# Kernel optimization log

Hardware: AMD Instinct MI355X
Metric: run time of the kernel (lower is better)

The kernel has to match this reference:

```python
import jax, jax.numpy as jnp
import numpy as np


def setup_inputs() -> dict:
    key = jax.random.key(0)
    k1, k2, k3 = jax.random.split(key, 3)
    num, c_in, c_out, nx, ny, din, dout = 128, 3, 8, 31, 31, 4, 6
    x = jax.random.normal(k1, (num, c_in, din, nx + 1, ny + 1), dtype=jnp.float32)
    tensors = jax.random.normal(k2, (c_in, c_out, nx, ny, din, din, din, din, dout), dtype=jnp.float32)
    bias = jax.random.normal(k3, (c_out, nx, ny, dout), dtype=jnp.float32) * 1e-8
    return {"x": x, "tensors": tensors, "bias": bias}


def reference(x, tensors, bias):
    # x: [num, c_in, din, sx, sy]; tensors: [c_in, c_out, nx, ny, din,din,din,din, dout]
    num, c_in, din, sx, sy = x.shape
    X, Y = sx - 1, sy - 1  # == nx, ny
    c_out, dout = tensors.shape[1], tensors.shape[-1]
    # four 2x2-patch corners, each [num, c_in, din, X, Y]
    a = x[:, :, :, :-1, :-1]
    b = x[:, :, :, 1:, :-1]
    c = x[:, :, :, :-1, 1:]
    d = x[:, :, :, 1:, 1:]
    # outer product of the four corner vectors -> rank-4 local feature [num, c_in, din^4, X, Y]
    ab = jnp.einsum('ncixy,ncjxy->ncijxy', a, b)
    cd = jnp.einsum('nckxy,nclxy->ncklxy', c, d)
    patch = jnp.einsum('ncijxy,ncklxy->ncijklxy', ab, cd)
    patch = patch.reshape(num, c_in, din ** 4, X, Y)
    # per-position weight: [c_in, c_out, X, Y, din^4, dout]
    w = tensors.reshape(c_in, c_out, X, Y, din ** 4, dout)
    out = jnp.einsum('ncmxy,cpxymo->npoxy', patch, w)  # [num, c_out, dout, X, Y]
    out = out + bias.transpose(0, 3, 1, 2)[None]  # bias -> [1, c_out, dout, X, Y]
    return out
```

## Files before the change

### kernel.cpp

```cpp
#include <hip/hip_runtime.h>


typedef __attribute__((ext_vector_type(8))) short short8;
typedef __attribute__((ext_vector_type(4))) float floatx4;
typedef __attribute__((ext_vector_type(4))) unsigned int uintx4;

#define WS_ELEMS (961u * 6144u)
#define SA_STR 72
#define SW_STR 72

static __device__ __forceinline__ unsigned short f2bf(float f) {
  union { float f; unsigned u; } v; v.f = f;
  unsigned r = v.u + 0x7FFFu + ((v.u >> 16) & 1u);
  return (unsigned short)(r >> 16);
}

template <bool TO_WS>
__global__ __launch_bounds__(256, 4)
void ttn_conv_mfma(const float* __restrict__ x,
                   const float* __restrict__ tensors,
                   const float* __restrict__ bias,
                   float* __restrict__ dst) {
  __shared__ __align__(16) unsigned short sA[128 * SA_STR];
  __shared__ __align__(16) unsigned short sW[48 * SW_STR];

  const int site = blockIdx.x;
  const int xx = site / 31, yy = site - xx * 31;
  const int t = threadIdx.x;
  const int lane = t & 63, wave = t >> 6;
  const int row = lane & 15, quad = lane >> 4;

  const int n_st = t & 127;
  const int h = t >> 7;
  const int p_st = t >> 5;
  const int q_st = t & 31;

  floatx4 acc[2][3];
#pragma unroll
  for (int i0 = 0; i0 < 2; ++i0)
#pragma unroll
    for (int j0 = 0; j0 < 3; ++j0)
      acc[i0][j0] = (floatx4){0.f, 0.f, 0.f, 0.f};

  float areg[4], b0 = 0.f, b1 = 0.f, cdreg[16];
  float4 wv0, wv1, wv2;

  {
    const float* src = tensors + ((size_t)(p_st * 961 + site)) * 1536 + 12 * q_st;
    wv0 = *(const float4*)src;
    wv1 = *(const float4*)(src + 4);
    wv2 = *(const float4*)(src + 8);
  }

#pragma unroll
  for (int ch = 0; ch < 12; ++ch) {
    const int mb = ch & 3;
    if ((ch & 3) == 0) {
      const int c = ch >> 2;
      const float* xp = x + ((size_t)n_st * 3 + c) * 4096 + xx * 32 + yy;
      float bq[4], cq[4], dq[4];
#pragma unroll
      for (int i = 0; i < 4; ++i) {
        const float* r0 = xp + i * 1024;
        areg[i] = r0[0];
        cq[i]   = r0[1];
        bq[i]   = r0[32];
        dq[i]   = r0[33];
      }
      b0 = h ? bq[2] : bq[0];
      b1 = h ? bq[3] : bq[1];
#pragma unroll
      for (int k2 = 0; k2 < 4; ++k2)
#pragma unroll
        for (int l2 = 0; l2 < 4; ++l2)
          cdreg[k2 * 4 + l2] = cq[k2] * dq[l2];
    }
    __syncthreads();

    {
      const float vv[12] = {wv0.x, wv0.y, wv0.z, wv0.w, wv1.x, wv1.y,
                            wv1.z, wv1.w, wv2.x, wv2.y, wv2.z, wv2.w};
#pragma unroll
      for (int o = 0; o < 6; ++o) {
        const unsigned pk = (unsigned)f2bf(vv[o]) | ((unsigned)f2bf(vv[o + 6]) << 16);
        *(unsigned*)&sW[(p_st * 6 + o) * SW_STR + 2 * q_st] = pk;
      }
    }
#pragma unroll
    for (int e = 0; e < 2; ++e) {
      const float ab = areg[mb] * (e ? b1 : b0);
      unsigned pk[8];
#pragma unroll
      for (int u = 0; u < 8; ++u)
        pk[u] = (unsigned)f2bf(ab * cdreg[2 * u]) |
                ((unsigned)f2bf(ab * cdreg[2 * u + 1]) << 16);
      uintx4* dp = (uintx4*)&sA[n_st * SA_STR + (2 * h + e) * 16];
      uintx4 v0 = {pk[0], pk[1], pk[2], pk[3]};
      uintx4 v1 = {pk[4], pk[5], pk[6], pk[7]};
      dp[0] = v0;
      dp[1] = v1;
    }
    if (ch < 11) {
      const int cn = (ch + 1) >> 2, mbn = (ch + 1) & 3;
      const float* src = tensors +
          ((size_t)((cn * 8 + p_st) * 961 + site)) * 1536 + (mbn * 64 + 2 * q_st) * 6;
      wv0 = *(const float4*)src;
      wv1 = *(const float4*)(src + 4);
      wv2 = *(const float4*)(src + 8);
    }
    __syncthreads();

#pragma unroll
    for (int ks = 0; ks < 2; ++ks) {
      const int kof = ks * 32 + quad * 8;
      short8 af[2], bf[3];
#pragma unroll
      for (int mt = 0; mt < 2; ++mt)
        af[mt] = *(const short8*)&sA[(wave * 32 + mt * 16 + row) * SA_STR + kof];
#pragma unroll
      for (int nt = 0; nt < 3; ++nt)
        bf[nt] = *(const short8*)&sW[(nt * 16 + row) * SW_STR + kof];
#pragma unroll
      for (int mt = 0; mt < 2; ++mt)
#pragma unroll
        for (int nt = 0; nt < 3; ++nt)
          acc[mt][nt] = __builtin_amdgcn_mfma_f32_16x16x32_bf16(
              af[mt], bf[nt], acc[mt][nt], 0, 0, 0);
    }
  }

  if (TO_WS) {
#pragma unroll
    for (int mt = 0; mt < 2; ++mt)
#pragma unroll
      for (int r = 0; r < 4; ++r) {
        const int n = wave * 32 + mt * 16 + quad * 4 + r;
#pragma unroll
        for (int nt = 0; nt < 3; ++nt) {
          const int po = nt * 16 + row;
          dst[(size_t)site * 6144 + n * 48 + po] = acc[mt][nt][r];
        }
      }
  } else {
#pragma unroll
    for (int mt = 0; mt < 2; ++mt)
#pragma unroll
      for (int r = 0; r < 4; ++r) {
        const int n = wave * 32 + mt * 16 + quad * 4 + r;
#pragma unroll
        for (int nt = 0; nt < 3; ++nt) {
          const int po = nt * 16 + row;
          const int p = po / 6, o = po - p * 6;
          dst[(size_t)(n * 48 + po) * 961 + site] =
              acc[mt][nt][r] + bias[(p * 961 + site) * 6 + o];
        }
      }
  }
}

__global__ __launch_bounds__(256, 8)
void ttn_transpose_bias(const float* __restrict__ ws,
                        const float* __restrict__ bias,
                        float* __restrict__ out) {
  __shared__ float tile[32][33];
  const int f0 = blockIdx.x * 32;
  const int s0 = blockIdx.y * 32;
  const int tx = threadIdx.x;
  const int ty = threadIdx.y;

#pragma unroll
  for (int rr = 0; rr < 4; ++rr) {
    const int srow = ty + rr * 8;
    const int site = s0 + srow;
    if (site < 961)
      tile[srow][tx] = ws[(size_t)site * 6144 + f0 + tx];
  }
  __syncthreads();

#pragma unroll
  for (int rr = 0; rr < 4; ++rr) {
    const int fy = ty + rr * 8;
    const int f = f0 + fy;
    const int site = s0 + tx;
    if (site < 961) {
      const int po = f % 48;
      const int p = po / 6, o = po - p * 6;
      out[(size_t)f * 961 + site] = tile[tx][fy] + bias[(p * 961 + site) * 6 + o];
    }
  }
}

extern "C" void kernel_launch(void* const* d_in, const int* in_sizes, int n_in,
                              void* d_out, int out_size, void* d_ws, size_t ws_size,
                              hipStream_t stream) {
  const float* x       = (const float*)d_in[0];
  const float* tensors = (const float*)d_in[1];
  const float* bias    = (const float*)d_in[2];
  float* out           = (float*)d_out;

  const size_t need = (size_t)WS_ELEMS * sizeof(float);
  if (d_ws != nullptr && ws_size >= need) {
    float* ws = (float*)d_ws;
    hipLaunchKernelGGL((ttn_conv_mfma<true>), dim3(961), dim3(256), 0, stream,
                       x, tensors, bias, ws);
    hipLaunchKernelGGL(ttn_transpose_bias, dim3(192, 31), dim3(32, 8), 0, stream,
                       ws, bias, out);
  } else {
    hipLaunchKernelGGL((ttn_conv_mfma<false>), dim3(961), dim3(256), 0, stream,
                       x, tensors, bias, out);
  }
}
```

Baseline: 244.8 us.

## Build patch A-fragments in registers and double-buffer weight tiles in LDS

The shared-memory staging of the outer-product patch matrix is removed. Each lane now computes its own bf16 A-fragment directly in registers from per-row corner values that it loads itself. Weight tiles are double-buffered in LDS, which leaves one barrier per chunk instead of two and overlaps weight loading with the MFMA work. Conversion switches to the packed HIP bf16 intrinsic. In exchange the factor loads are duplicated across lanes, there are more uncoalesced x reads, and register pressure rises.

```diff
diff --git a/kernel.cpp b/kernel.cpp
--- a/kernel.cpp
+++ b/kernel.cpp
@@ -1,18 +1,18 @@
 #include <hip/hip_runtime.h>
+#include <hip/hip_bf16.h>
 
 
 typedef __attribute__((ext_vector_type(8))) short short8;
 typedef __attribute__((ext_vector_type(4))) float floatx4;
-typedef __attribute__((ext_vector_type(4))) unsigned int uintx4;
 
 #define WS_ELEMS (961u * 6144u)
-#define SA_STR 72
 #define SW_STR 72
 
-static __device__ __forceinline__ unsigned short f2bf(float f) {
-  union { float f; unsigned u; } v; v.f = f;
-  unsigned r = v.u + 0x7FFFu + ((v.u >> 16) & 1u);
-  return (unsigned short)(r >> 16);
+static __device__ __forceinline__ unsigned pkbf(float lo, float hi) {
+  __hip_bfloat162 h = __float22bfloat162_rn(make_float2(lo, hi));
+  union { __hip_bfloat162 h; unsigned u; } v;
+  v.h = h;
+  return v.u;
 }
 
 template <bool TO_WS>
@@ -21,8 +21,7 @@
                    const float* __restrict__ tensors,
                    const float* __restrict__ bias,
                    float* __restrict__ dst) {
-  __shared__ __align__(16) unsigned short sA[128 * SA_STR];
-  __shared__ __align__(16) unsigned short sW[48 * SW_STR];
+  __shared__ __align__(16) unsigned short sW[2][48 * SW_STR];
 
   const int site = blockIdx.x;
   const int xx = site / 31, yy = site - xx * 31;
@@ -30,10 +29,7 @@
   const int lane = t & 63, wave = t >> 6;
   const int row = lane & 15, quad = lane >> 4;
 
-  const int n_st = t & 127;
-  const int h = t >> 7;
-  const int p_st = t >> 5;
-  const int q_st = t & 31;
+  const int p_st = t >> 5, q_st = t & 31;
 
   floatx4 acc[2][3];
 #pragma unroll
@@ -42,90 +38,82 @@
     for (int j0 = 0; j0 < 3; ++j0)
       acc[i0][j0] = (floatx4){0.f, 0.f, 0.f, 0.f};
 
-  float areg[4], b0 = 0.f, b1 = 0.f, cdreg[16];
+  float a4[2][4], b2[2][2], cd8[2][8];
   float4 wv0, wv1, wv2;
 
-  {
-    const float* src = tensors + ((size_t)(p_st * 961 + site)) * 1536 + 12 * q_st;
+  auto loadW = [&](int c, int mb) {
+    const float* src = tensors +
+        ((size_t)((c * 8 + p_st) * 961 + site)) * 1536 + (size_t)(mb * 64 + 2 * q_st) * 6;
     wv0 = *(const float4*)src;
     wv1 = *(const float4*)(src + 4);
     wv2 = *(const float4*)(src + 8);
-  }
-
-#pragma unroll
-  for (int ch = 0; ch < 12; ++ch) {
-    const int mb = ch & 3;
-    if ((ch & 3) == 0) {
-      const int c = ch >> 2;
-      const float* xp = x + ((size_t)n_st * 3 + c) * 4096 + xx * 32 + yy;
-      float bq[4], cq[4], dq[4];
+  };
+  auto storeW = [&](int buf) {
+    const float vv[12] = {wv0.x, wv0.y, wv0.z, wv0.w, wv1.x, wv1.y,
+                          wv1.z, wv1.w, wv2.x, wv2.y, wv2.z, wv2.w};
+#pragma unroll
+    for (int o = 0; o < 6; ++o)
+      *(unsigned*)&sW[buf][(p_st * 6 + o) * SW_STR + 2 * q_st] = pkbf(vv[o], vv[o + 6]);
+  };
+  auto loadFactors = [&](int c) {
+#pragma unroll
+    for (int mt = 0; mt < 2; ++mt) {
+      const int n = wave * 32 + mt * 16 + row;
+      const float* xb = x + ((size_t)n * 3 + c) * 4096 + xx * 32 + yy;
+      float dq[4];
 #pragma unroll
       for (int i = 0; i < 4; ++i) {
-        const float* r0 = xp + i * 1024;
-        areg[i] = r0[0];
-        cq[i]   = r0[1];
-        bq[i]   = r0[32];
-        dq[i]   = r0[33];
-      }
-      b0 = h ? bq[2] : bq[0];
-      b1 = h ? bq[3] : bq[1];
-#pragma unroll
-      for (int k2 = 0; k2 < 4; ++k2)
-#pragma unroll
-        for (int l2 = 0; l2 < 4; ++l2)
-          cdreg[k2 * 4 + l2] = cq[k2] * dq[l2];
+        a4[mt][i] = xb[i * 1024];
+        dq[i]     = xb[i * 1024 + 33];
+      }
+      b2[mt][0] = xb[(quad >> 1) * 1024 + 32];
+      b2[mt][1] = xb[(2 + (quad >> 1)) * 1024 + 32];
+      const float cq0 = xb[(2 * (quad & 1)) * 1024 + 1];
+      const float cq1 = xb[(2 * (quad & 1) + 1) * 1024 + 1];
+#pragma unroll
+      for (int j = 0; j < 8; ++j)
+        cd8[mt][j] = (j < 4 ? cq0 : cq1) * dq[j & 3];
     }
-    __syncthreads();
-
-    {
-      const float vv[12] = {wv0.x, wv0.y, wv0.z, wv0.w, wv1.x, wv1.y,
-                            wv1.z, wv1.w, wv2.x, wv2.y, wv2.z, wv2.w};
-#pragma unroll
-      for (int o = 0; o < 6; ++o) {
-        const unsigned pk = (unsigned)f2bf(vv[o]) | ((unsigned)f2bf(vv[o + 6]) << 16);
-        *(unsigned*)&sW[(p_st * 6 + o) * SW_STR + 2 * q_st] = pk;
-      }
-    }
-#pragma unroll
-    for (int e = 0; e < 2; ++e) {
-      const float ab = areg[mb] * (e ? b1 : b0);
-      unsigned pk[8];
-#pragma unroll
-      for (int u = 0; u < 8; ++u)
-        pk[u] = (unsigned)f2bf(ab * cdreg[2 * u]) |
-                ((unsigned)f2bf(ab * cdreg[2 * u + 1]) << 16);
-      uintx4* dp = (uintx4*)&sA[n_st * SA_STR + (2 * h + e) * 16];
-      uintx4 v0 = {pk[0], pk[1], pk[2], pk[3]};
-      uintx4 v1 = {pk[4], pk[5], pk[6], pk[7]};
-      dp[0] = v0;
-      dp[1] = v1;
-    }
-    if (ch < 11) {
-      const int cn = (ch + 1) >> 2, mbn = (ch + 1) & 3;
-      const float* src = tensors +
-          ((size_t)((cn * 8 + p_st) * 961 + site)) * 1536 + (mbn * 64 + 2 * q_st) * 6;
-      wv0 = *(const float4*)src;
-      wv1 = *(const float4*)(src + 4);
-      wv2 = *(const float4*)(src + 8);
-    }
-    __syncthreads();
-
-#pragma unroll
-    for (int ks = 0; ks < 2; ++ks) {
-      const int kof = ks * 32 + quad * 8;
-      short8 af[2], bf[3];
-#pragma unroll
-      for (int mt = 0; mt < 2; ++mt)
-        af[mt] = *(const short8*)&sA[(wave * 32 + mt * 16 + row) * SA_STR + kof];
-#pragma unroll
-      for (int nt = 0; nt < 3; ++nt)
-        bf[nt] = *(const short8*)&sW[(nt * 16 + row) * SW_STR + kof];
-#pragma unroll
-      for (int mt = 0; mt < 2; ++mt)
+  };
+
+  loadW(0, 0);
+  storeW(0);
+  loadW(0, 1);
+  loadFactors(0);
+
+  for (int c = 0; c < 3; ++c) {
+    if (c) loadFactors(c);
+#pragma unroll
+    for (int mb = 0; mb < 4; ++mb) {
+      const int ch = c * 4 + mb;
+      const int bp = mb & 1;
+      __syncthreads();
+
+#pragma unroll
+      for (int ks = 0; ks < 2; ++ks) {
+        short8 bfr[3];
 #pragma unroll
         for (int nt = 0; nt < 3; ++nt)
-          acc[mt][nt] = __builtin_amdgcn_mfma_f32_16x16x32_bf16(
-              af[mt], bf[nt], acc[mt][nt], 0, 0, 0);
+          bfr[nt] = *(const short8*)&sW[bp][(nt * 16 + row) * SW_STR + ks * 32 + quad * 8];
+#pragma unroll
+        for (int mt = 0; mt < 2; ++mt) {
+          const float ab = a4[mt][mb] * b2[mt][ks];
+          union { unsigned u[4]; short8 s; } af;
+#pragma unroll
+          for (int jj = 0; jj < 4; ++jj)
+            af.u[jj] = pkbf(ab * cd8[mt][2 * jj], ab * cd8[mt][2 * jj + 1]);
+#pragma unroll
+          for (int nt = 0; nt < 3; ++nt)
+            acc[mt][nt] = __builtin_amdgcn_mfma_f32_16x16x32_bf16(
+                af.s, bfr[nt], acc[mt][nt], 0, 0, 0);
+        }
+      }
+
+      if (ch < 11) storeW(1 - bp);
+      if (ch < 10) {
+        const int i2 = ch + 2;
+        loadW(i2 >> 2, i2 & 3);
+      }
     }
   }
 
```

Result: slower. 255.4 us (+4.4%).
